# Kernel tuning notes

Hardware: AMD Instinct MI355X
Metric: run time of the kernel (lower is better)

The kernel has to match this reference:

```python
import jax, jax.numpy as jnp
import numpy as np

B, N, D = 2, 2048, 768
H = 12
HD = D // H
SCALE = HD ** -0.5
EPS = 1e-8


def exp0(v, c):
    # Poincare exponential map at origin: tanh(sqrt(c)||v||) * v / (sqrt(c)||v||)
    sc = jnp.sqrt(c)
    n = jnp.sqrt(jnp.sum(v * v, axis=-1, keepdims=True))
    n = jnp.maximum(n, EPS)
    return jnp.tanh(sc * n) * v / (sc * n)


def log0(x, c):
    # Poincare log map at origin: artanh(sqrt(c)||x||) * x / (sqrt(c)||x||)
    sc = jnp.sqrt(c)
    n = jnp.sqrt(jnp.sum(x * x, axis=-1, keepdims=True))
    n = jnp.maximum(n, EPS)
    t = jnp.clip(sc * n, 0.0, 1.0 - 1e-7)
    return jnp.arctanh(t) * x / (sc * n)


def setup_inputs() -> dict:
    key = jax.random.key(0)
    k1, k2, k3 = jax.random.split(key, 3)
    c0 = 0.1
    x = jax.random.normal(k1, (B, N, D), dtype=jnp.float32)
    # rescale so sqrt(c)*||x|| = 0.5 -> valid points strictly inside the ball
    xn = jnp.sqrt(jnp.sum(x * x, axis=-1, keepdims=True))
    x = x * (0.5 / (np.sqrt(c0) * jnp.maximum(xn, EPS)))
    w_qkv = jax.random.normal(k2, (3 * D, D), dtype=jnp.float32) * (D ** -0.5)
    w_proj = jax.random.normal(k3, (D, D), dtype=jnp.float32) * (D ** -0.5)
    b_proj = jnp.zeros((D,), dtype=jnp.float32)
    curvature = jnp.asarray(c0, dtype=jnp.float32)
    return {"x": x, "w_qkv": w_qkv, "w_proj": w_proj, "b_proj": b_proj,
            "curvature": curvature}


def reference(x, w_qkv, w_proj, b_proj, curvature):
    c = curvature
    v = log0(x, c)                                   # [B,N,D] tangent vectors
    qkv = jnp.einsum('bnd,ed->bne', v, w_qkv)        # [B,N,3D]
    qkv = qkv.reshape(B, N, 3, H, HD).transpose(2, 0, 3, 1, 4)  # [3,B,H,N,HD]
    q, k, v_proj = qkv[0], qkv[1], qkv[2]
    # Map q,k back onto the manifold for the hyperbolic distance score
    qm = exp0(q, c)                                  # [B,H,N,HD]
    km = exp0(k, c)
    q_nsq = jnp.sum(qm * qm, axis=-1)                # [B,H,N]
    k_nsq = jnp.sum(km * km, axis=-1)                # [B,H,N]
    dot = jnp.einsum('bhnd,bhmd->bhnm', qm, km)      # [B,H,N,N]
    # ||q-k||^2 = ||q||^2 + ||k||^2 - 2 q.k  (avoids [B,H,N,N,HD] intermediate)
    diff_sq = jnp.maximum(q_nsq[..., :, None] + k_nsq[..., None, :] - 2.0 * dot, 0.0)
    q_cl = jnp.minimum(q_nsq, 0.99)
    k_cl = jnp.minimum(k_nsq, 0.99)
    denom = (1.0 - q_cl)[..., :, None] * (1.0 - k_cl)[..., None, :] + 1e-8
    inner = jnp.maximum(1.0 + 2.0 * diff_sq / denom, 1.0 + 1e-7)
    distances = jnp.arccosh(inner)                   # [B,H,N,N]
    scores = -distances * SCALE
    attn = jax.nn.softmax(scores, axis=-1)
    out = jnp.einsum('bhnm,bhmd->bhnd', attn, v_proj)
    out = out.transpose(0, 2, 1, 3).reshape(B, N, D)
    v_out = jnp.einsum('bnd,ed->bne', out, w_proj) + b_proj
    return exp0(v_out, c)                            # [B,N,D] on manifold
```

## Files before the change

### kernel.cpp

```cpp
#include <hip/hip_runtime.h>
#include <cmath>

#define ROWS 4096
#define DIM 768
#define QKV_COLS 2304
#define NHEAD 12
#define HEAD_DIM 64
#define SEQ 2048
#define PADK 72

static constexpr float SCALE_F = 0.125f;
static constexpr float EPS_F   = 1e-8f;

typedef __bf16 bfrag __attribute__((ext_vector_type(8)));
typedef float  f32x4 __attribute__((ext_vector_type(4)));

__device__ __forceinline__ float wave_sum64(float v) {
#pragma unroll
  for (int off = 1; off < 64; off <<= 1) v += __shfl_xor(v, off, 64);
  return v;
}

__device__ __forceinline__ unsigned short f2bf(float f) {
  unsigned u = __float_as_uint(f);
  u += 0x7fffu + ((u >> 16) & 1u);
  return (unsigned short)(u >> 16);
}

__device__ __forceinline__ void gl_lds16(const void* g, void* l) {
  __builtin_amdgcn_global_load_lds((const __attribute__((address_space(1))) void*)g,
                                   (__attribute__((address_space(3))) void*)l, 16, 0, 0);
}

__global__ __launch_bounds__(256) void conv_bf16_2(const float* __restrict__ a, int na,
                                                   const float* __restrict__ b, int nb,
                                                   unsigned short* __restrict__ da,
                                                   unsigned short* __restrict__ db) {
  const int i = (blockIdx.x * 256 + threadIdx.x) * 4;
  const float* s;
  unsigned short* d;
  int j;
  if (i < na) { s = a; d = da; j = i; }
  else { j = i - na; if (j >= nb) return; s = b; d = db; }
  const float4 v = *(const float4*)(s + j);
  ushort4 o;
  o.x = f2bf(v.x); o.y = f2bf(v.y); o.z = f2bf(v.z); o.w = f2bf(v.w);
  *(ushort4*)(d + j) = o;
}

__global__ __launch_bounds__(256) void log0_kernel(const float* __restrict__ x,
                                                   const float* __restrict__ cptr,
                                                   unsigned short* __restrict__ vout) {
  const int lane = threadIdx.x & 63;
  const int row  = (blockIdx.x << 2) + (threadIdx.x >> 6);
  const float* xr = x + (size_t)row * DIM;
  unsigned short* vr = vout + (size_t)row * DIM;
  float vals[12];
  float ss = 0.f;
#pragma unroll
  for (int i = 0; i < 12; ++i) {
    float t = xr[lane + (i << 6)];
    vals[i] = t;
    ss += t * t;
  }
  ss = wave_sum64(ss);
  const float sc  = sqrtf(cptr[0]);
  const float n   = fmaxf(sqrtf(ss), EPS_F);
  const float scn = sc * n;
  const float t   = fminf(scn, 1.0f - 1e-7f);
  const float f   = atanhf(t) / scn;
#pragma unroll
  for (int i = 0; i < 12; ++i) vr[lane + (i << 6)] = f2bf(vals[i] * f);
}

__global__ __launch_bounds__(256) void exp0_out_kernel(const float* __restrict__ vin,
                                                       const float* __restrict__ cptr,
                                                       float* __restrict__ outp) {
  const int lane = threadIdx.x & 63;
  const int row  = (blockIdx.x << 2) + (threadIdx.x >> 6);
  const float* vr = vin + (size_t)row * DIM;
  float* orow = outp + (size_t)row * DIM;
  float vals[12];
  float ss = 0.f;
#pragma unroll
  for (int i = 0; i < 12; ++i) {
    float t = vr[lane + (i << 6)];
    vals[i] = t;
    ss += t * t;
  }
  ss = wave_sum64(ss);
  const float sc  = sqrtf(cptr[0]);
  const float n   = fmaxf(sqrtf(ss), EPS_F);
  const float scn = sc * n;
  const float f   = tanhf(scn) / scn;
#pragma unroll
  for (int i = 0; i < 12; ++i) orow[lane + (i << 6)] = vals[i] * f;
}

__global__ __launch_bounds__(256) void gemm_nt_mfma(const unsigned short* __restrict__ A,
                                                    const unsigned short* __restrict__ B,
                                                    float* __restrict__ C,
                                                    int M, int Ncols, int K,
                                                    const float* __restrict__ bias) {
  __shared__ unsigned short As[128 * 32];
  __shared__ unsigned short Bs[128 * 32];
  const int tid = threadIdx.x;
  const int w = tid >> 6, lane = tid & 63;
  const int lq = lane & 15, quad = lane >> 4;
  const int wr = w >> 1, wc = w & 1;
  const int row0 = blockIdx.y << 7;
  const int col0 = blockIdx.x << 7;

  const int srow  = lane >> 2;
  const int skoff = (lane & 3) << 3;

  f32x4 acc[4][4];
#pragma unroll
  for (int i = 0; i < 4; ++i)
#pragma unroll
    for (int j = 0; j < 4; ++j) acc[i][j] = (f32x4){0.f, 0.f, 0.f, 0.f};

  for (int k0 = 0; k0 < K; k0 += 32) {
    __syncthreads();
#pragma unroll
    for (int q = 0; q < 2; ++q) {
      const int r = ((w << 1) + q) << 4;
      gl_lds16(A + (size_t)(row0 + r + srow) * K + k0 + skoff, &As[((w << 1) + q) << 9]);
      gl_lds16(B + (size_t)(col0 + r + srow) * K + k0 + skoff, &Bs[((w << 1) + q) << 9]);
    }
    __syncthreads();

    bfrag af[4], bfg[4];
#pragma unroll
    for (int i = 0; i < 4; ++i)
      af[i] = *(const bfrag*)&As[((wr << 6) + (i << 4) + lq) * 32 + (quad << 3)];
#pragma unroll
    for (int j = 0; j < 4; ++j)
      bfg[j] = *(const bfrag*)&Bs[((wc << 6) + (j << 4) + lq) * 32 + (quad << 3)];
#pragma unroll
    for (int i = 0; i < 4; ++i)
#pragma unroll
      for (int j = 0; j < 4; ++j)
        acc[i][j] = __builtin_amdgcn_mfma_f32_16x16x32_bf16(af[i], bfg[j], acc[i][j], 0, 0, 0);
  }

#pragma unroll
  for (int i = 0; i < 4; ++i) {
    const int crow = row0 + (wr << 6) + (i << 4) + (quad << 2);
#pragma unroll
    for (int j = 0; j < 4; ++j) {
      const int col = col0 + (wc << 6) + (j << 4) + lq;
      const float bj = bias ? bias[col] : 0.0f;
      float* cp = C + (size_t)crow * Ncols + col;
#pragma unroll
      for (int r = 0; r < 4; ++r)
        cp[(size_t)r * Ncols] = acc[i][j][r] + bj;
    }
  }
}

__global__ __launch_bounds__(256) void qkv_prep(const float* __restrict__ qkv,
                                                const float* __restrict__ cptr,
                                                unsigned short* __restrict__ qh,
                                                unsigned short* __restrict__ kh,
                                                unsigned short* __restrict__ vth,
                                                float2* __restrict__ qn2,
                                                float2* __restrict__ kn2) {
  const int qt = blockIdx.x, h = blockIdx.y, b = blockIdx.z;
  const int bh = b * NHEAD + h;
  const int tid = threadIdx.x;
  const int w = tid >> 6, lane = tid & 63;
  const float sc = sqrtf(cptr[0]);

  for (int t = 0; t < 32; ++t) {
    const int vv = w * 32 + t;
    const int which = vv & 1;
    const int r = vv >> 1;
    const int n = qt * 64 + r;
    const float v = qkv[((size_t)(b * SEQ + n)) * QKV_COLS + which * DIM + h * HEAD_DIM + lane];
    const float ss = wave_sum64(v * v);
    const float nn = fmaxf(sqrtf(ss), EPS_F);
    const float scn = sc * nn;
    const float f = tanhf(scn) / scn;
    (which ? kh : qh)[((size_t)bh * SEQ + n) * HEAD_DIM + lane] = f2bf(v * f);
    if (lane == 0) {
      const float nrm = ss * f * f;
      (which ? kn2 : qn2)[(size_t)bh * SEQ + n] =
          make_float2(nrm, 1.0f / (1.0f - fminf(nrm, 0.99f)));
    }
  }

  __shared__ unsigned short T[64 * PADK];
  const int r2 = tid >> 2;
  const int c0 = (tid & 3) << 4;
  const float* src = qkv + ((size_t)(b * SEQ + qt * 64 + r2)) * QKV_COLS + 2 * DIM + h * HEAD_DIM + c0;
#pragma unroll
  for (int z = 0; z < 16; z += 4) {
    const float4 v = *(const float4*)(src + z);
    T[(c0 + z + 0) * PADK + r2] = f2bf(v.x);
    T[(c0 + z + 1) * PADK + r2] = f2bf(v.y);
    T[(c0 + z + 2) * PADK + r2] = f2bf(v.z);
    T[(c0 + z + 3) * PADK + r2] = f2bf(v.w);
  }
  __syncthreads();
  const int d  = tid >> 2;
  const int k0 = (tid & 3) << 4;
  unsigned short* dst = vth + ((size_t)bh * HEAD_DIM + d) * SEQ + (size_t)qt * 64 + k0;
  *(uint4*)dst       = *(const uint4*)&T[d * PADK + k0];
  *(uint4*)(dst + 8) = *(const uint4*)&T[d * PADK + k0 + 8];
}

__global__ __launch_bounds__(256) void flash_mfma(const unsigned short* __restrict__ qh,
                                                  const unsigned short* __restrict__ kh,
                                                  const unsigned short* __restrict__ vth,
                                                  const float2* __restrict__ qn2,
                                                  const float2* __restrict__ kn2,
                                                  unsigned short* __restrict__ attn_out) {
  const int qt = blockIdx.x, h = blockIdx.y, b = blockIdx.z;
  const int bh = b * NHEAD + h;
  const int tid = threadIdx.x;
  const int w = tid >> 6, lane = tid & 63;
  const int lq = lane & 15, quad = lane >> 4;

  __shared__ unsigned short Ks[2 * 64 * 64];
  __shared__ unsigned short Vt[2 * 64 * 64];
  __shared__ unsigned short Ps[64 * PADK];
  __shared__ float knA[128], knB[128];
  __shared__ float l_s[64];

  const unsigned short* qbase = qh + ((size_t)bh * SEQ + (size_t)qt * 64) * HEAD_DIM;
  const float2* qnb = qn2 + (size_t)bh * SEQ + (size_t)qt * 64;
  const float2* knb = kn2 + (size_t)bh * SEQ;

  const int srow = tid >> 3, spos = tid & 7;
  const int sB = spos ^ (srow & 7);
  const char* kgsrc = (const char*)(kh + (size_t)bh * SEQ * HEAD_DIM) + (size_t)srow * 128 + sB * 16;
  const char* vgsrc = (const char*)(vth + (size_t)bh * HEAD_DIM * SEQ) + (size_t)srow * 4096 + sB * 16;

  bfrag aq[2];
#pragma unroll
  for (int khf = 0; khf < 2; ++khf)
    aq[khf] = *(const bfrag*)(qbase + (size_t)(w * 16 + lq) * HEAD_DIM + khf * 32 + quad * 8);

  const float2 qq = qnb[w * 16 + lq];
  const float qnS = qq.x;
  const float rqS = 2.0f * qq.y;

  f32x4 oacc[4];
#pragma unroll
  for (int d = 0; d < 4; ++d) oacc[d] = (f32x4){0.f, 0.f, 0.f, 0.f};
  float l = 0.0f;
  const int swz = lq & 7;

  for (int rd = 0; rd < SEQ / 128; ++rd) {
    __syncthreads();
    gl_lds16(kgsrc,                (char*)Ks + w * 1024);
    gl_lds16(kgsrc + 4096,         (char*)Ks + 4096 + w * 1024);
    gl_lds16(kgsrc + 8192,         (char*)Ks + 8192 + w * 1024);
    gl_lds16(kgsrc + 12288,        (char*)Ks + 12288 + w * 1024);
    gl_lds16(vgsrc,                (char*)Vt + w * 1024);
    gl_lds16(vgsrc + 131072,       (char*)Vt + 4096 + w * 1024);
    gl_lds16(vgsrc + 128,          (char*)Vt + 8192 + w * 1024);
    gl_lds16(vgsrc + 131072 + 128, (char*)Vt + 12288 + w * 1024);
    if (tid < 128) {
      const float2 kv = knb[rd * 128 + tid];
      knA[tid] = kv.x;
      knB[tid] = kv.y;
    }
    kgsrc += 16384;
    vgsrc += 256;
    __syncthreads();

#pragma unroll
    for (int t = 0; t < 2; ++t) {
      const unsigned short* KsT = &Ks[t * 4096];
      const unsigned short* VtT = &Vt[t * 4096];

      f32x4 s[4];
#pragma unroll
      for (int st = 0; st < 4; ++st) s[st] = (f32x4){0.f, 0.f, 0.f, 0.f};
#pragma unroll
      for (int khf = 0; khf < 2; ++khf)
#pragma unroll
        for (int st = 0; st < 4; ++st) {
          const bfrag ak = *(const bfrag*)&KsT[(st * 16 + lq) * 64 + (((khf << 2) + quad) ^ swz) * 8];
          s[st] = __builtin_amdgcn_mfma_f32_16x16x32_bf16(ak, aq[khf], s[st], 0, 0, 0);
        }

#pragma unroll
      for (int st = 0; st < 4; ++st) {
        const f32x4 kna = *(const f32x4*)&knA[t * 64 + st * 16 + quad * 4];
        const f32x4 knr = *(const f32x4*)&knB[t * 64 + st * 16 + quad * 4];
        unsigned u[4];
#pragma unroll
        for (int i = 0; i < 4; ++i) {
          float tt = fmaf(-2.0f, s[st][i], qnS + kna[i]);
          tt = fmaxf(tt, 0.0f);
          const float inner = fmaf(tt, rqS * knr[i], 1.0f);
          const float root = __builtin_amdgcn_sqrtf(fmaf(inner, inner, -1.0f));
          const float wgt = __builtin_amdgcn_exp2f(-0.125f * __builtin_amdgcn_logf(inner + root));
          u[i] = __float_as_uint(wgt);
          l += __uint_as_float(u[i] & 0xffff0000u);
        }
        uint2 pk;
        pk.x = (u[0] >> 16) | (u[1] & 0xffff0000u);
        pk.y = (u[2] >> 16) | (u[3] & 0xffff0000u);
        *(uint2*)&Ps[(w * 16 + lq) * PADK + st * 16 + quad * 4] = pk;
      }

#pragma unroll
      for (int khf = 0; khf < 2; ++khf) {
        const bfrag ap = *(const bfrag*)&Ps[(w * 16 + lq) * PADK + khf * 32 + quad * 8];
#pragma unroll
        for (int d = 0; d < 4; ++d) {
          const bfrag bv = *(const bfrag*)&VtT[(d * 16 + lq) * 64 + (((khf << 2) + quad) ^ swz) * 8];
          oacc[d] = __builtin_amdgcn_mfma_f32_16x16x32_bf16(ap, bv, oacc[d], 0, 0, 0);
        }
      }
    }
  }

  l += __shfl_xor(l, 16, 64);
  l += __shfl_xor(l, 32, 64);
  if (quad == 0) l_s[w * 16 + lq] = l;
  float rl4[4];
#pragma unroll
  for (int i = 0; i < 4; ++i) rl4[i] = __builtin_amdgcn_rcpf(l_s[w * 16 + quad * 4 + i]);

  unsigned short* ob = attn_out + ((size_t)b * SEQ + (size_t)qt * 64 + w * 16) * DIM + h * HEAD_DIM;
#pragma unroll
  for (int d = 0; d < 4; ++d)
#pragma unroll
    for (int i = 0; i < 4; ++i)
      ob[(size_t)(quad * 4 + i) * DIM + d * 16 + lq] = f2bf(oacc[d][i] * rl4[i]);
}

extern "C" void kernel_launch(void* const* d_in, const int* in_sizes, int n_in,
                              void* d_out, int out_size, void* d_ws, size_t ws_size,
                              hipStream_t stream) {
  const float* x      = (const float*)d_in[0];
  const float* w_qkv  = (const float*)d_in[1];
  const float* w_proj = (const float*)d_in[2];
  const float* b_proj = (const float*)d_in[3];
  const float* curv   = (const float*)d_in[4];
  float* outp = (float*)d_out;

  float* ws = (float*)d_ws;
  unsigned short* v_tan_bf = (unsigned short*)ws;
  unsigned short* attn_bf  = (unsigned short*)ws;
  float* qkv   = ws + 1572864;
  float* v_out = qkv;
  unsigned short* qh  = (unsigned short*)(qkv + 9437184);
  unsigned short* kh  = qh + 3145728;
  unsigned short* vth = kh + 3145728;
  unsigned short* wqkv_bf  = vth + 3145728;
  unsigned short* wproj_bf = wqkv_bf + 1769472;
  float2* qn2 = (float2*)(wproj_bf + 589824);
  float2* kn2 = qn2 + 49152;

  conv_bf16_2<<<dim3((2359296 / 4 + 255) / 256), dim3(256), 0, stream>>>(
      w_qkv, 1769472, w_proj, 589824, wqkv_bf, wproj_bf);
  log0_kernel<<<dim3(ROWS / 4), dim3(256), 0, stream>>>(x, curv, v_tan_bf);
  gemm_nt_mfma<<<dim3(QKV_COLS / 128, ROWS / 128), dim3(256), 0, stream>>>(
      v_tan_bf, wqkv_bf, qkv, ROWS, QKV_COLS, DIM, nullptr);
  qkv_prep<<<dim3(SEQ / 64, NHEAD, 2), dim3(256), 0, stream>>>(qkv, curv, qh, kh, vth,
                                                               qn2, kn2);
  flash_mfma<<<dim3(SEQ / 64, NHEAD, 2), dim3(256), 0, stream>>>(qh, kh, vth, qn2,
                                                                 kn2, attn_bf);
  gemm_nt_mfma<<<dim3(DIM / 128, ROWS / 128), dim3(256), 0, stream>>>(
      attn_bf, wproj_bf, v_out, ROWS, DIM, DIM, b_proj);
  exp0_out_kernel<<<dim3(ROWS / 4), dim3(256), 0, stream>>>(v_out, curv, outp);
}
```

Measured before the change: 234.5 us.

## Double-buffer LDS tiles in GEMM and flash attention to overlap loads with compute

The GEMM kernel becomes a template with two LDS buffers. The next K-slice is prefetched right after a single barrier, so its loads overlap the MFMA work on the current slice. The output projection now uses 64x64 tiles, launching more blocks for the small-N GEMM. The flash kernel switches from 128-key rounds with two barriers to 64-key tiles that are double-buffered with one barrier per tile, and packs bf16 pairs with a byte-permute instruction. The trade-off is twice the LDS per buffer and reliance on the barrier draining outstanding async LDS loads before a buffer is read.

```diff
diff --git a/kernel.cpp b/kernel.cpp
--- a/kernel.cpp
+++ b/kernel.cpp
@@ -97,59 +97,68 @@
   for (int i = 0; i < 12; ++i) orow[lane + (i << 6)] = vals[i] * f;
 }
 
-__global__ __launch_bounds__(256) void gemm_nt_mfma(const unsigned short* __restrict__ A,
+template<int BM, int BN>
+__global__ __launch_bounds__(256) void gemm_nt_dbuf(const unsigned short* __restrict__ A,
                                                     const unsigned short* __restrict__ B,
                                                     float* __restrict__ C,
                                                     int M, int Ncols, int K,
                                                     const float* __restrict__ bias) {
-  __shared__ unsigned short As[128 * 32];
-  __shared__ unsigned short Bs[128 * 32];
+  constexpr int FI = BM / 32;
+  constexpr int FJ = BN / 32;
+  constexpr int CH = BM / 64;
+  __shared__ unsigned short As[2][BM * 32];
+  __shared__ unsigned short Bs[2][BN * 32];
   const int tid = threadIdx.x;
   const int w = tid >> 6, lane = tid & 63;
   const int lq = lane & 15, quad = lane >> 4;
   const int wr = w >> 1, wc = w & 1;
-  const int row0 = blockIdx.y << 7;
-  const int col0 = blockIdx.x << 7;
-
+  const int row0 = blockIdx.y * BM;
+  const int col0 = blockIdx.x * BN;
   const int srow  = lane >> 2;
   const int skoff = (lane & 3) << 3;
 
-  f32x4 acc[4][4];
-#pragma unroll
-  for (int i = 0; i < 4; ++i)
-#pragma unroll
-    for (int j = 0; j < 4; ++j) acc[i][j] = (f32x4){0.f, 0.f, 0.f, 0.f};
-
-  for (int k0 = 0; k0 < K; k0 += 32) {
+  f32x4 acc[FI][FJ];
+#pragma unroll
+  for (int i = 0; i < FI; ++i)
+#pragma unroll
+    for (int j = 0; j < FJ; ++j) acc[i][j] = (f32x4){0.f, 0.f, 0.f, 0.f};
+
+  auto pf = [&](int k0, int buf) {
+#pragma unroll
+    for (int c = 0; c < CH; ++c) {
+      const int r = c * 64 + w * 16;
+      gl_lds16(A + (size_t)(row0 + r + srow) * K + k0 + skoff, &As[buf][r * 32]);
+      gl_lds16(B + (size_t)(col0 + r + srow) * K + k0 + skoff, &Bs[buf][r * 32]);
+    }
+  };
+
+  pf(0, 0);
+  const int NIT = K / 32;
+  for (int it = 0; it < NIT; ++it) {
+    const int buf = it & 1;
     __syncthreads();
-#pragma unroll
-    for (int q = 0; q < 2; ++q) {
-      const int r = ((w << 1) + q) << 4;
-      gl_lds16(A + (size_t)(row0 + r + srow) * K + k0 + skoff, &As[((w << 1) + q) << 9]);
-      gl_lds16(B + (size_t)(col0 + r + srow) * K + k0 + skoff, &Bs[((w << 1) + q) << 9]);
-    }
-    __syncthreads();
-
-    bfrag af[4], bfg[4];
-#pragma unroll
-    for (int i = 0; i < 4; ++i)
-      af[i] = *(const bfrag*)&As[((wr << 6) + (i << 4) + lq) * 32 + (quad << 3)];
-#pragma unroll
-    for (int j = 0; j < 4; ++j)
-      bfg[j] = *(const bfrag*)&Bs[((wc << 6) + (j << 4) + lq) * 32 + (quad << 3)];
-#pragma unroll
-    for (int i = 0; i < 4; ++i)
-#pragma unroll
-      for (int j = 0; j < 4; ++j)
+    if (it + 1 < NIT) pf((it + 1) * 32, buf ^ 1);
+
+    bfrag af[FI], bfg[FJ];
+#pragma unroll
+    for (int i = 0; i < FI; ++i)
+      af[i] = *(const bfrag*)&As[buf][(wr * (BM / 2) + i * 16 + lq) * 32 + (quad << 3)];
+#pragma unroll
+    for (int j = 0; j < FJ; ++j)
+      bfg[j] = *(const bfrag*)&Bs[buf][(wc * (BN / 2) + j * 16 + lq) * 32 + (quad << 3)];
+#pragma unroll
+    for (int i = 0; i < FI; ++i)
+#pragma unroll
+      for (int j = 0; j < FJ; ++j)
         acc[i][j] = __builtin_amdgcn_mfma_f32_16x16x32_bf16(af[i], bfg[j], acc[i][j], 0, 0, 0);
   }
 
 #pragma unroll
-  for (int i = 0; i < 4; ++i) {
-    const int crow = row0 + (wr << 6) + (i << 4) + (quad << 2);
-#pragma unroll
-    for (int j = 0; j < 4; ++j) {
-      const int col = col0 + (wc << 6) + (j << 4) + lq;
+  for (int i = 0; i < FI; ++i) {
+    const int crow = row0 + wr * (BM / 2) + i * 16 + (quad << 2);
+#pragma unroll
+    for (int j = 0; j < FJ; ++j) {
+      const int col = col0 + wc * (BN / 2) + j * 16 + lq;
       const float bj = bias ? bias[col] : 0.0f;
       float* cp = C + (size_t)crow * Ncols + col;
 #pragma unroll
@@ -222,10 +231,10 @@
   const int w = tid >> 6, lane = tid & 63;
   const int lq = lane & 15, quad = lane >> 4;
 
-  __shared__ unsigned short Ks[2 * 64 * 64];
-  __shared__ unsigned short Vt[2 * 64 * 64];
+  __shared__ unsigned short Ks[2][64 * 64];
+  __shared__ unsigned short Vt[2][64 * 64];
   __shared__ unsigned short Ps[64 * PADK];
-  __shared__ float knA[128], knB[128];
+  __shared__ float knA[2][64], knB[2][64];
   __shared__ float l_s[64];
 
   const unsigned short* qbase = qh + ((size_t)bh * SEQ + (size_t)qt * 64) * HEAD_DIM;
@@ -237,6 +246,20 @@
   const char* kgsrc = (const char*)(kh + (size_t)bh * SEQ * HEAD_DIM) + (size_t)srow * 128 + sB * 16;
   const char* vgsrc = (const char*)(vth + (size_t)bh * HEAD_DIM * SEQ) + (size_t)srow * 4096 + sB * 16;
 
+  auto prefetch = [&](int kt, int buf) {
+    const char* kp = kgsrc + (size_t)kt * 8192;
+    const char* vp = vgsrc + (size_t)kt * 128;
+    gl_lds16(kp,          (char*)Ks[buf] + w * 1024);
+    gl_lds16(kp + 4096,   (char*)Ks[buf] + 4096 + w * 1024);
+    gl_lds16(vp,          (char*)Vt[buf] + w * 1024);
+    gl_lds16(vp + 131072, (char*)Vt[buf] + 4096 + w * 1024);
+    if (tid < 64) {
+      const float2 kv = knb[kt * 64 + tid];
+      knA[buf][tid] = kv.x;
+      knB[buf][tid] = kv.y;
+    }
+  };
+
   bfrag aq[2];
 #pragma unroll
   for (int khf = 0; khf < 2; ++khf)
@@ -252,70 +275,51 @@
   float l = 0.0f;
   const int swz = lq & 7;
 
-  for (int rd = 0; rd < SEQ / 128; ++rd) {
+  prefetch(0, 0);
+  for (int kt = 0; kt < SEQ / 64; ++kt) {
+    const int buf = kt & 1;
     __syncthreads();
-    gl_lds16(kgsrc,                (char*)Ks + w * 1024);
-    gl_lds16(kgsrc + 4096,         (char*)Ks + 4096 + w * 1024);
-    gl_lds16(kgsrc + 8192,         (char*)Ks + 8192 + w * 1024);
-    gl_lds16(kgsrc + 12288,        (char*)Ks + 12288 + w * 1024);
-    gl_lds16(vgsrc,                (char*)Vt + w * 1024);
-    gl_lds16(vgsrc + 131072,       (char*)Vt + 4096 + w * 1024);
-    gl_lds16(vgsrc + 128,          (char*)Vt + 8192 + w * 1024);
-    gl_lds16(vgsrc + 131072 + 128, (char*)Vt + 12288 + w * 1024);
-    if (tid < 128) {
-      const float2 kv = knb[rd * 128 + tid];
-      knA[tid] = kv.x;
-      knB[tid] = kv.y;
-    }
-    kgsrc += 16384;
-    vgsrc += 256;
-    __syncthreads();
-
-#pragma unroll
-    for (int t = 0; t < 2; ++t) {
-      const unsigned short* KsT = &Ks[t * 4096];
-      const unsigned short* VtT = &Vt[t * 4096];
-
-      f32x4 s[4];
-#pragma unroll
-      for (int st = 0; st < 4; ++st) s[st] = (f32x4){0.f, 0.f, 0.f, 0.f};
-#pragma unroll
-      for (int khf = 0; khf < 2; ++khf)
-#pragma unroll
-        for (int st = 0; st < 4; ++st) {
-          const bfrag ak = *(const bfrag*)&KsT[(st * 16 + lq) * 64 + (((khf << 2) + quad) ^ swz) * 8];
-          s[st] = __builtin_amdgcn_mfma_f32_16x16x32_bf16(ak, aq[khf], s[st], 0, 0, 0);
-        }
-
+    if (kt + 1 < SEQ / 64) prefetch(kt + 1, buf ^ 1);
+
+    f32x4 s[4];
+#pragma unroll
+    for (int st = 0; st < 4; ++st) s[st] = (f32x4){0.f, 0.f, 0.f, 0.f};
+#pragma unroll
+    for (int khf = 0; khf < 2; ++khf)
 #pragma unroll
       for (int st = 0; st < 4; ++st) {
-        const f32x4 kna = *(const f32x4*)&knA[t * 64 + st * 16 + quad * 4];
-        const f32x4 knr = *(const f32x4*)&knB[t * 64 + st * 16 + quad * 4];
-        unsigned u[4];
-#pragma unroll
-        for (int i = 0; i < 4; ++i) {
-          float tt = fmaf(-2.0f, s[st][i], qnS + kna[i]);
-          tt = fmaxf(tt, 0.0f);
-          const float inner = fmaf(tt, rqS * knr[i], 1.0f);
-          const float root = __builtin_amdgcn_sqrtf(fmaf(inner, inner, -1.0f));
-          const float wgt = __builtin_amdgcn_exp2f(-0.125f * __builtin_amdgcn_logf(inner + root));
-          u[i] = __float_as_uint(wgt);
-          l += __uint_as_float(u[i] & 0xffff0000u);
-        }
-        uint2 pk;
-        pk.x = (u[0] >> 16) | (u[1] & 0xffff0000u);
-        pk.y = (u[2] >> 16) | (u[3] & 0xffff0000u);
-        *(uint2*)&Ps[(w * 16 + lq) * PADK + st * 16 + quad * 4] = pk;
+        const bfrag ak = *(const bfrag*)&Ks[buf][(st * 16 + lq) * 64 + (((khf << 2) + quad) ^ swz) * 8];
+        s[st] = __builtin_amdgcn_mfma_f32_16x16x32_bf16(ak, aq[khf], s[st], 0, 0, 0);
       }
 
 #pragma unroll
-      for (int khf = 0; khf < 2; ++khf) {
-        const bfrag ap = *(const bfrag*)&Ps[(w * 16 + lq) * PADK + khf * 32 + quad * 8];
-#pragma unroll
-        for (int d = 0; d < 4; ++d) {
-          const bfrag bv = *(const bfrag*)&VtT[(d * 16 + lq) * 64 + (((khf << 2) + quad) ^ swz) * 8];
-          oacc[d] = __builtin_amdgcn_mfma_f32_16x16x32_bf16(ap, bv, oacc[d], 0, 0, 0);
-        }
+    for (int st = 0; st < 4; ++st) {
+      const f32x4 kna = *(const f32x4*)&knA[buf][st * 16 + quad * 4];
+      const f32x4 knr = *(const f32x4*)&knB[buf][st * 16 + quad * 4];
+      unsigned u[4];
+#pragma unroll
+      for (int i = 0; i < 4; ++i) {
+        float tt = fmaf(-2.0f, s[st][i], qnS + kna[i]);
+        tt = fmaxf(tt, 0.0f);
+        const float inner = fmaf(tt, rqS * knr[i], 1.0f);
+        const float root = __builtin_amdgcn_sqrtf(fmaf(inner, inner, -1.0f));
+        const float wgt = __builtin_amdgcn_exp2f(-0.125f * __builtin_amdgcn_logf(inner + root));
+        u[i] = __float_as_uint(wgt);
+        l += __uint_as_float(u[i] & 0xffff0000u);
+      }
+      uint2 pk;
+      pk.x = __builtin_amdgcn_perm(u[1], u[0], 0x07060302u);
+      pk.y = __builtin_amdgcn_perm(u[3], u[2], 0x07060302u);
+      *(uint2*)&Ps[(w * 16 + lq) * PADK + st * 16 + quad * 4] = pk;
+    }
+
+#pragma unroll
+    for (int khf = 0; khf < 2; ++khf) {
+      const bfrag ap = *(const bfrag*)&Ps[(w * 16 + lq) * PADK + khf * 32 + quad * 8];
+#pragma unroll
+      for (int d = 0; d < 4; ++d) {
+        const bfrag bv = *(const bfrag*)&Vt[buf][(d * 16 + lq) * 64 + (((khf << 2) + quad) ^ swz) * 8];
+        oacc[d] = __builtin_amdgcn_mfma_f32_16x16x32_bf16(ap, bv, oacc[d], 0, 0, 0);
       }
     }
   }
@@ -361,13 +365,13 @@
   conv_bf16_2<<<dim3((2359296 / 4 + 255) / 256), dim3(256), 0, stream>>>(
       w_qkv, 1769472, w_proj, 589824, wqkv_bf, wproj_bf);
   log0_kernel<<<dim3(ROWS / 4), dim3(256), 0, stream>>>(x, curv, v_tan_bf);
-  gemm_nt_mfma<<<dim3(QKV_COLS / 128, ROWS / 128), dim3(256), 0, stream>>>(
+  gemm_nt_dbuf<128, 128><<<dim3(QKV_COLS / 128, ROWS / 128), dim3(256), 0, stream>>>(
       v_tan_bf, wqkv_bf, qkv, ROWS, QKV_COLS, DIM, nullptr);
   qkv_prep<<<dim3(SEQ / 64, NHEAD, 2), dim3(256), 0, stream>>>(qkv, curv, qh, kh, vth,
                                                                qn2, kn2);
   flash_mfma<<<dim3(SEQ / 64, NHEAD, 2), dim3(256), 0, stream>>>(qh, kh, vth, qn2,
                                                                  kn2, attn_bf);
-  gemm_nt_mfma<<<dim3(DIM / 128, ROWS / 128), dim3(256), 0, stream>>>(
+  gemm_nt_dbuf<64, 64><<<dim3(DIM / 64, ROWS / 64), dim3(256), 0, stream>>>(
       attn_bf, wproj_bf, v_out, ROWS, DIM, DIM, b_proj);
   exp0_out_kernel<<<dim3(ROWS / 4), dim3(256), 0, stream>>>(v_out, curv, outp);
 }
```

Result: faster. 227.1 us (-3.1%).
